# Kernel tuning notes

Measured on AMD Instinct MI355X. Metric: run time of the kernel, lower is better.

The kernel has to match this reference:

```python
import jax, jax.numpy as jnp
import numpy as np

B, N, C = 2, 4096, 1024
H, D = 16, 64
EPS = 1e-6


def setup_inputs() -> dict:
    key = jax.random.key(0)
    k1, k2, k3 = jax.random.split(key, 3)
    hidden_states = jax.random.normal(k1, (B, N, C), dtype=jnp.float32)
    # realistic RoPE tables: inv_freq over half-dim, duplicated to full head_dim
    half = D // 2
    inv_freq = 1.0 / (10000.0 ** (jnp.arange(half, dtype=jnp.float32) / half))
    t = jnp.arange(N, dtype=jnp.float32)
    freqs = jnp.outer(t, inv_freq)                     # [N, D/2]
    emb = jnp.concatenate([freqs, freqs], axis=-1)     # [N, D]
    cos, sin = jnp.cos(emb), jnp.sin(emb)
    Wqkv = jax.random.normal(k2, (C, 3 * C), dtype=jnp.float32) * (C ** -0.5)
    Wout = jax.random.normal(k3, (C, C), dtype=jnp.float32) * (C ** -0.5)
    gq = jnp.ones((D,), dtype=jnp.float32)
    gk = jnp.ones((D,), dtype=jnp.float32)
    return {"hidden_states": hidden_states, "cos": cos, "sin": sin,
            "Wqkv": Wqkv, "Wout": Wout, "gq": gq, "gk": gk}


def _rmsnorm(x, g):
    # normalize over last dim (head_dim)
    var = jnp.mean(jnp.square(x), axis=-1, keepdims=True)
    return x * jax.lax.rsqrt(var + EPS) * g


def _rotate_half(x):
    x1, x2 = jnp.split(x, 2, axis=-1)
    return jnp.concatenate([-x2, x1], axis=-1)


def reference(hidden_states, cos, sin, Wqkv, Wout, gq, gk):
    b, n, c = hidden_states.shape
    qkv = (hidden_states @ Wqkv).reshape(b, n, 3, H, D)
    qkv = jnp.transpose(qkv, (2, 0, 3, 1, 4))
    q, k, v = qkv[0], qkv[1], qkv[2]
    # per-head RMSNorm on q/k
    q = _rmsnorm(q, gq)
    k = _rmsnorm(k, gk)
    # RoPE: cos/sin [N,D] broadcast to [B,H,N,D]
    q = q * cos + _rotate_half(q) * sin
    k = k * cos + _rotate_half(k) * sin
    # full SDPA (flex_attention with no block_mask/score_mod)
    scale = D ** -0.5
    scores = jnp.einsum("bhqd,bhkd->bhqk", q, k) * scale
    probs = jax.nn.softmax(scores, axis=-1)
    attn = jnp.einsum("bhqk,bhkd->bhqd", probs, v)
    attn = jnp.transpose(attn, (0, 2, 1, 3)).reshape(b, n, c)
    return attn @ Wout
```

## Files before the change

### kernel.cpp

```cpp
#include <hip/hip_runtime.h>
#include <hip/hip_bf16.h>
#include <stdint.h>

#define LOG2E 1.44269504088896340736f

typedef __attribute__((ext_vector_type(8))) short short8;
typedef __attribute__((ext_vector_type(4))) float f32x4;
typedef __attribute__((ext_vector_type(16))) float f32x16;
typedef __attribute__((ext_vector_type(4))) unsigned short us4;

static __device__ __forceinline__ float bf2f(unsigned short u) {
    union { unsigned int i; float f; } v; v.i = ((unsigned int)u) << 16; return v.f;
}
static __device__ __forceinline__ unsigned short f2bf(float f) {
    __hip_bfloat16 h = __float2bfloat16(f);
    union { __hip_bfloat16 h; unsigned short u; } v; v.h = h; return v.u;
}

#define GLL(gsrc, ldst) \
    __builtin_amdgcn_global_load_lds((const __attribute__((address_space(1))) unsigned int*)(gsrc), \
                                     (__attribute__((address_space(3))) unsigned int*)(ldst), 16, 0, 0)

__global__ __launch_bounds__(256) void conv_bf16(const float4* __restrict__ in,
                                                 us4* __restrict__ out, int n4) {
    int i = blockIdx.x * blockDim.x + threadIdx.x;
    int stride = gridDim.x * blockDim.x;
    for (; i < n4; i += stride) {
        float4 v = in[i];
        us4 o;
        o[0] = f2bf(v.x); o[1] = f2bf(v.y); o[2] = f2bf(v.z); o[3] = f2bf(v.w);
        out[i] = o;
    }
}

__global__ __launch_bounds__(256) void transpose_w(const float* __restrict__ W,
                                                   unsigned short* __restrict__ WT,
                                                   int K, int M) {
    __shared__ unsigned short T[64][65];
    int m0 = blockIdx.x * 64, k0 = blockIdx.y * 64;
    int r = threadIdx.x >> 2, q = (threadIdx.x & 3) * 16;
    const float4* src = (const float4*)(W + (size_t)(k0 + r) * M + m0 + q);
#pragma unroll
    for (int j = 0; j < 4; j++) {
        float4 v = src[j];
        T[r][q + j * 4 + 0] = f2bf(v.x);
        T[r][q + j * 4 + 1] = f2bf(v.y);
        T[r][q + j * 4 + 2] = f2bf(v.z);
        T[r][q + j * 4 + 3] = f2bf(v.w);
    }
    __syncthreads();
    unsigned short tmp[16];
#pragma unroll
    for (int j = 0; j < 16; j++) tmp[j] = T[q + j][r];
    unsigned short* dst = WT + (size_t)(m0 + r) * K + k0 + q;
    *(short8*)dst = *(const short8*)tmp;
    *(short8*)(dst + 8) = *(const short8*)(tmp + 8);
}

__device__ __forceinline__ void gemm_core(const unsigned short* __restrict__ A,
                                          const unsigned short* __restrict__ Bt,
                                          int brow, int bcol,
                                          unsigned short* As, unsigned short* Bs,
                                          f32x4 (&acc)[4][4]) {
    const int tid = threadIdx.x;
    const int w = tid >> 6, lane = tid & 63;
    const int g = lane >> 4, c = lane & 15;
    const int wr = (w >> 1) * 64, wc = (w & 1) * 64;

    for (int k0 = 0; k0 < 1024; k0 += 64) {
        __syncthreads();
#pragma unroll
        for (int i = 0; i < 4; i++) {
            int slot = i * 256 + tid;
            int row = slot >> 3, sub = slot & 7;
            int koff = k0 + ((sub ^ (row & 7)) << 3);
            GLL(A + (size_t)(brow + row) * 1024 + koff, As + (size_t)(i * 256 + w * 64) * 8);
            GLL(Bt + (size_t)(bcol + row) * 1024 + koff, Bs + (size_t)(i * 256 + w * 64) * 8);
        }
        __syncthreads();
#pragma unroll
        for (int kc = 0; kc < 2; kc++) {
            short8 a[4], b[4];
#pragma unroll
            for (int f = 0; f < 4; f++) {
                int rowA = wr + f * 16 + c;
                a[f] = *(const short8*)(As + (size_t)(rowA * 8 + ((kc * 4 + g) ^ (rowA & 7))) * 8);
                int rowB = wc + f * 16 + c;
                b[f] = *(const short8*)(Bs + (size_t)(rowB * 8 + ((kc * 4 + g) ^ (rowB & 7))) * 8);
            }
#pragma unroll
            for (int fi = 0; fi < 4; fi++)
#pragma unroll
                for (int fj = 0; fj < 4; fj++)
                    acc[fi][fj] = __builtin_amdgcn_mfma_f32_16x16x32_bf16(a[fi], b[fj], acc[fi][fj], 0, 0, 0);
        }
    }
}

__global__ __launch_bounds__(256) void gemm_qkv(const unsigned short* __restrict__ A,
                                                const unsigned short* __restrict__ Bt,
                                                unsigned short* __restrict__ qkv,
                                                unsigned short* __restrict__ vt) {
    __shared__ unsigned short As[128 * 64];
    __shared__ unsigned short Bs[128 * 64];
    const int tid = threadIdx.x;
    const int lane = tid & 63, w = tid >> 6;
    const int g = lane >> 4, c = lane & 15;
    const int brow = blockIdx.x * 128, bcol = blockIdx.y * 128;
    const int wr = (w >> 1) * 64, wc = (w & 1) * 64;

    f32x4 acc[4][4];
#pragma unroll
    for (int i = 0; i < 4; i++)
#pragma unroll
        for (int j = 0; j < 4; j++) acc[i][j] = (f32x4){0.f, 0.f, 0.f, 0.f};

    gemm_core(A, Bt, brow, bcol, As, Bs, acc);

    if (bcol < 2048) {
#pragma unroll
        for (int fi = 0; fi < 4; fi++) {
            int row = brow + wr + fi * 16 + g * 4;
#pragma unroll
            for (int fj = 0; fj < 4; fj++) {
                int col = bcol + wc + fj * 16 + c;
#pragma unroll
                for (int r = 0; r < 4; r++)
                    qkv[(size_t)(row + r) * 2048 + col] = f2bf(acc[fi][fj][r]);
            }
        }
    } else {
        int b = brow >> 12;
        int nbase = (brow & 4095) + wr;
#pragma unroll
        for (int fi = 0; fi < 4; fi++) {
            int n0 = nbase + fi * 16 + g * 4;
#pragma unroll
            for (int fj = 0; fj < 4; fj++) {
                int hd = bcol - 2048 + wc + fj * 16 + c;
                us4 pk;
#pragma unroll
                for (int r = 0; r < 4; r++) pk[r] = f2bf(acc[fi][fj][r]);
                *(us4*)(vt + (size_t)(b * 1024 + hd) * 4096 + n0) = pk;
            }
        }
    }
}

__global__ __launch_bounds__(256) void gemm_out(const unsigned short* __restrict__ A,
                                                const unsigned short* __restrict__ Bt,
                                                float* __restrict__ C) {
    __shared__ unsigned short As[128 * 64];
    __shared__ unsigned short Bs[128 * 64];
    const int tid = threadIdx.x;
    const int lane = tid & 63, w = tid >> 6;
    const int g = lane >> 4, c = lane & 15;
    const int brow = blockIdx.x * 128, bcol = blockIdx.y * 128;
    const int wr = (w >> 1) * 64, wc = (w & 1) * 64;

    f32x4 acc[4][4];
#pragma unroll
    for (int i = 0; i < 4; i++)
#pragma unroll
        for (int j = 0; j < 4; j++) acc[i][j] = (f32x4){0.f, 0.f, 0.f, 0.f};

    gemm_core(A, Bt, brow, bcol, As, Bs, acc);

#pragma unroll
    for (int fi = 0; fi < 4; fi++) {
        int row = brow + wr + fi * 16 + g * 4;
#pragma unroll
        for (int fj = 0; fj < 4; fj++) {
            int col = bcol + wc + fj * 16 + c;
#pragma unroll
            for (int r = 0; r < 4; r++)
                C[(size_t)(row + r) * 1024 + col] = acc[fi][fj][r];
        }
    }
}

__global__ __launch_bounds__(256) void norm_rope(unsigned short* __restrict__ qkv,
                                                 const float* __restrict__ cosb,
                                                 const float* __restrict__ sinb,
                                                 const float* __restrict__ gq,
                                                 const float* __restrict__ gk) {
    int u = blockIdx.x * 4 + (threadIdx.x >> 6);
    int lane = threadIdx.x & 63;
    int t = u >> 5, rest = u & 31, h = rest >> 1, qk = rest & 1;
    int n = t & 4095;
    unsigned short* p = qkv + (size_t)t * 2048 + qk * 1024 + h * 64 + lane;
    float x = bf2f(*p);
    float ss = x * x;
#pragma unroll
    for (int m = 1; m < 64; m <<= 1) ss += __shfl_xor(ss, m, 64);
    float rr = rsqrtf(ss * 0.015625f + 1e-6f);
    float xn = x * rr * (qk ? gk[lane] : gq[lane]);
    float other = __shfl_xor(xn, 32, 64);
    float cv = cosb[n * 64 + lane], sv = sinb[n * 64 + lane];
    float rh = (lane < 32) ? -other : other;
    *p = f2bf(xn * cv + rh * sv);
}

__global__ __launch_bounds__(256, 2) void attn_fwd(const unsigned short* __restrict__ qkv,
                                                   const unsigned short* __restrict__ vt,
                                                   unsigned short* __restrict__ attn) {
    __shared__ unsigned short Ks[2][4096];
    __shared__ unsigned short Vs[2][4096];
    const int tid = threadIdx.x;
    const int w = tid >> 6, lane = tid & 63;
    const int c31 = lane & 31, hi = lane >> 5;

    int logical = (blockIdx.x & 7) * 64 + (blockIdx.x >> 3);
    const int bh = logical >> 4, qt = logical & 15;
    const int b = bh >> 4, h = bh & 15;
    const size_t tokbase = (size_t)b * 4096;
    const int q0 = qt * 256 + w * 64;

    short8 qf[2][4];
#pragma unroll
    for (int qs = 0; qs < 2; qs++)
#pragma unroll
        for (int sl = 0; sl < 4; sl++) {
            const unsigned short* src =
                qkv + (tokbase + q0 + qs * 32 + c31) * 2048 + h * 64 + sl * 16 + hi * 8;
            short8 v = *(const short8*)src;
#pragma unroll
            for (int j = 0; j < 8; j++)
                v[j] = (short)f2bf(bf2f((unsigned short)v[j]) * 0.125f);
            qf[qs][sl] = v;
        }

    f32x16 o[2][2];
#pragma unroll
    for (int qs = 0; qs < 2; qs++)
#pragma unroll
        for (int ds = 0; ds < 2; ds++)
#pragma unroll
            for (int r = 0; r < 16; r++) o[qs][ds][r] = 0.f;
    float m_run[2] = {-__builtin_inff(), -__builtin_inff()};
    float l_run[2] = {0.f, 0.f};

#define STAGE_KV(bi, kv0)                                                                     \
    {                                                                                          \
        _Pragma("unroll") for (int i = 0; i < 2; i++) {                                        \
            int s2 = i * 4 + w;                                                                \
            GLL(qkv + (tokbase + (kv0) + lane) * 2048 + 1024 + h * 64 + s2 * 8,                \
                &Ks[bi][(size_t)s2 * 512]);                                                    \
            GLL(vt + ((size_t)(bh * 64 + lane)) * 4096 + (kv0) + s2 * 8,                       \
                &Vs[bi][(size_t)s2 * 512]);                                                    \
        }                                                                                      \
    }

    STAGE_KV(0, 0);
    int cur = 0;

    for (int t = 0; t < 64; t++) {
        __syncthreads();
        if (t < 63) STAGE_KV(cur ^ 1, (t + 1) * 64);

        short8 kf[2][4];
#pragma unroll
        for (int m = 0; m < 2; m++)
#pragma unroll
            for (int sl = 0; sl < 4; sl++)
                kf[m][sl] = *(const short8*)&Ks[cur][(size_t)(((sl * 2 + hi) * 64) + m * 32 + c31) * 8];

        f32x16 sacc[2][2];
        __builtin_amdgcn_s_setprio(1);
#pragma unroll
        for (int qs = 0; qs < 2; qs++)
#pragma unroll
            for (int m = 0; m < 2; m++) {
                f32x16 a;
#pragma unroll
                for (int r = 0; r < 16; r++) a[r] = 0.f;
#pragma unroll
                for (int sl = 0; sl < 4; sl++)
                    a = __builtin_amdgcn_mfma_f32_32x32x16_bf16(kf[m][sl], qf[qs][sl], a, 0, 0, 0);
                sacc[qs][m] = a;
            }
        __builtin_amdgcn_s_setprio(0);

        short8 pf[2][4];
#pragma unroll
        for (int qs = 0; qs < 2; qs++) {
            f32x16 t16;
#pragma unroll
            for (int r = 0; r < 16; r++) t16[r] = fmaxf(sacc[qs][0][r], sacc[qs][1][r]);
#pragma unroll
            for (int st = 8; st > 0; st >>= 1)
#pragma unroll
                for (int j = 0; j < st; j++) t16[j] = fmaxf(t16[j], t16[j + st]);
            float mx = fmaxf(t16[0], __shfl_xor(t16[0], 32, 64));

            if (__any(mx > m_run[qs] + 4.0f)) {
                float mn = fmaxf(m_run[qs], mx);
                float alpha = __builtin_amdgcn_exp2f((m_run[qs] - mn) * LOG2E);
                m_run[qs] = mn;
                l_run[qs] *= alpha;
#pragma unroll
                for (int ds = 0; ds < 2; ds++)
#pragma unroll
                    for (int r = 0; r < 16; r++) o[qs][ds][r] *= alpha;
            }
            float nb = -m_run[qs] * LOG2E;

#pragma unroll
            for (int m = 0; m < 2; m++)
#pragma unroll
                for (int r = 0; r < 16; r++)
                    sacc[qs][m][r] = __builtin_amdgcn_exp2f(fmaf(sacc[qs][m][r], LOG2E, nb));

#pragma unroll
            for (int r = 0; r < 16; r++) t16[r] = sacc[qs][0][r] + sacc[qs][1][r];
#pragma unroll
            for (int st = 8; st > 0; st >>= 1)
#pragma unroll
                for (int j = 0; j < st; j++) t16[j] += t16[j + st];
            l_run[qs] += t16[0] + __shfl_xor(t16[0], 32, 64);

#pragma unroll
            for (int m = 0; m < 2; m++) {
                unsigned int q2[8];
#pragma unroll
                for (int w8 = 0; w8 < 8; w8++) {
                    unsigned int r_;
                    asm("v_cvt_pk_bf16_f32 %0, %1, %2"
                        : "=v"(r_)
                        : "v"(sacc[qs][m][2 * w8]), "v"(sacc[qs][m][2 * w8 + 1]));
                    q2[w8] = r_;
                }
                unsigned int x0 = hi ? q2[0] : q2[2];
                unsigned int x1 = hi ? q2[1] : q2[3];
                unsigned int x2 = hi ? q2[4] : q2[6];
                unsigned int x3 = hi ? q2[5] : q2[7];
                unsigned int r0 = (unsigned int)__shfl_xor((int)x0, 32, 64);
                unsigned int r1 = (unsigned int)__shfl_xor((int)x1, 32, 64);
                unsigned int r2 = (unsigned int)__shfl_xor((int)x2, 32, 64);
                unsigned int r3 = (unsigned int)__shfl_xor((int)x3, 32, 64);
                union { unsigned int u[4]; short8 s; } f0, f1;
                f0.u[0] = hi ? r0 : q2[0];
                f0.u[1] = hi ? r1 : q2[1];
                f0.u[2] = hi ? q2[2] : r0;
                f0.u[3] = hi ? q2[3] : r1;
                f1.u[0] = hi ? r2 : q2[4];
                f1.u[1] = hi ? r3 : q2[5];
                f1.u[2] = hi ? q2[6] : r2;
                f1.u[3] = hi ? q2[7] : r3;
                pf[qs][2 * m] = f0.s;
                pf[qs][2 * m + 1] = f1.s;
            }
        }

        __builtin_amdgcn_s_setprio(1);
#pragma unroll
        for (int ds = 0; ds < 2; ds++)
#pragma unroll
            for (int kvs = 0; kvs < 4; kvs++) {
                short8 vf = *(const short8*)&Vs[cur][(size_t)(((kvs * 2 + hi) * 64) + ds * 32 + c31) * 8];
                o[0][ds] = __builtin_amdgcn_mfma_f32_32x32x16_bf16(vf, pf[0][kvs], o[0][ds], 0, 0, 0);
                o[1][ds] = __builtin_amdgcn_mfma_f32_32x32x16_bf16(vf, pf[1][kvs], o[1][ds], 0, 0, 0);
            }
        __builtin_amdgcn_s_setprio(0);
        cur ^= 1;
    }

#pragma unroll
    for (int qs = 0; qs < 2; qs++) {
        float inv = 1.f / l_run[qs];
        int token = q0 + qs * 32 + c31;
#pragma unroll
        for (int ds = 0; ds < 2; ds++)
#pragma unroll
            for (int rb = 0; rb < 4; rb++) {
                us4 pk;
#pragma unroll
                for (int j = 0; j < 4; j++) pk[j] = f2bf(o[qs][ds][rb * 4 + j] * inv);
                *(us4*)(attn + (tokbase + token) * 1024 + h * 64 + ds * 32 + rb * 8 + hi * 4) = pk;
            }
    }
#undef STAGE_KV
}

extern "C" void kernel_launch(void* const* d_in, const int* in_sizes, int n_in,
                              void* d_out, int out_size, void* d_ws, size_t ws_size,
                              hipStream_t stream) {
    const float* hs   = (const float*)d_in[0];
    const float* cosb = (const float*)d_in[1];
    const float* sinb = (const float*)d_in[2];
    const float* wqkv = (const float*)d_in[3];
    const float* wout = (const float*)d_in[4];
    const float* gq   = (const float*)d_in[5];
    const float* gk   = (const float*)d_in[6];
    float* out = (float*)d_out;

    char* ws = (char*)d_ws;
    unsigned short* Xb    = (unsigned short*)(ws);
    unsigned short* WqkvT = (unsigned short*)(ws + 16777216);
    unsigned short* WoutT = (unsigned short*)(ws + 23068672);
    unsigned short* qkv   = (unsigned short*)(ws + 25165824);
    unsigned short* vt    = (unsigned short*)(ws + 58720256);
    unsigned short* attn  = (unsigned short*)(ws + 75497472);

    conv_bf16<<<4096, 256, 0, stream>>>((const float4*)hs, (us4*)Xb, (8192 * 1024) / 4);
    transpose_w<<<dim3(48, 16), 256, 0, stream>>>(wqkv, WqkvT, 1024, 3072);
    transpose_w<<<dim3(16, 16), 256, 0, stream>>>(wout, WoutT, 1024, 1024);
    gemm_qkv<<<dim3(64, 24), 256, 0, stream>>>(Xb, WqkvT, qkv, vt);
    norm_rope<<<65536, 256, 0, stream>>>(qkv, cosb, sinb, gq, gk);
    attn_fwd<<<512, 256, 0, stream>>>(qkv, vt, attn);
    gemm_out<<<dim3(64, 8), 256, 0, stream>>>(attn, WoutT, out);
}
```

Measured before the change: 419.1 us.

## Halve attention query tile per wave to double blocks and occupancy

Each wave now handles 32 query rows instead of 64, so a block covers 128 queries and the grid doubles to 1024 blocks, with launch bounds raised to 4 blocks per CU. The smaller per-wave state (Q fragments, O accumulators, scores) cuts register pressure so more waves can hide latency, and the larger grid fills the 256 CUs more evenly. In exchange, each staged K/V tile is reused by half as many queries, which doubles K/V global and LDS traffic per unit of compute and lowers MFMA work per LDS read.

```diff
diff --git a/kernel.cpp b/kernel.cpp
--- a/kernel.cpp
+++ b/kernel.cpp
@@ -201,7 +201,7 @@
     *p = f2bf(xn * cv + rh * sv);
 }
 
-__global__ __launch_bounds__(256, 2) void attn_fwd(const unsigned short* __restrict__ qkv,
+__global__ __launch_bounds__(256, 4) void attn_fwd(const unsigned short* __restrict__ qkv,
                                                    const unsigned short* __restrict__ vt,
                                                    unsigned short* __restrict__ attn) {
     __shared__ unsigned short Ks[2][4096];
@@ -210,35 +210,31 @@
     const int w = tid >> 6, lane = tid & 63;
     const int c31 = lane & 31, hi = lane >> 5;
 
-    int logical = (blockIdx.x & 7) * 64 + (blockIdx.x >> 3);
-    const int bh = logical >> 4, qt = logical & 15;
+    int logical = (blockIdx.x & 7) * 128 + (blockIdx.x >> 3);
+    const int bh = logical >> 5, qt = logical & 31;
     const int b = bh >> 4, h = bh & 15;
     const size_t tokbase = (size_t)b * 4096;
-    const int q0 = qt * 256 + w * 64;
-
-    short8 qf[2][4];
-#pragma unroll
-    for (int qs = 0; qs < 2; qs++)
-#pragma unroll
-        for (int sl = 0; sl < 4; sl++) {
-            const unsigned short* src =
-                qkv + (tokbase + q0 + qs * 32 + c31) * 2048 + h * 64 + sl * 16 + hi * 8;
-            short8 v = *(const short8*)src;
-#pragma unroll
-            for (int j = 0; j < 8; j++)
-                v[j] = (short)f2bf(bf2f((unsigned short)v[j]) * 0.125f);
-            qf[qs][sl] = v;
-        }
-
-    f32x16 o[2][2];
-#pragma unroll
-    for (int qs = 0; qs < 2; qs++)
-#pragma unroll
-        for (int ds = 0; ds < 2; ds++)
-#pragma unroll
-            for (int r = 0; r < 16; r++) o[qs][ds][r] = 0.f;
-    float m_run[2] = {-__builtin_inff(), -__builtin_inff()};
-    float l_run[2] = {0.f, 0.f};
+    const int q0 = qt * 128 + w * 32;
+
+    short8 qf[4];
+#pragma unroll
+    for (int sl = 0; sl < 4; sl++) {
+        const unsigned short* src =
+            qkv + (tokbase + q0 + c31) * 2048 + h * 64 + sl * 16 + hi * 8;
+        short8 v = *(const short8*)src;
+#pragma unroll
+        for (int j = 0; j < 8; j++)
+            v[j] = (short)f2bf(bf2f((unsigned short)v[j]) * 0.125f);
+        qf[sl] = v;
+    }
+
+    f32x16 o[2];
+#pragma unroll
+    for (int ds = 0; ds < 2; ds++)
+#pragma unroll
+        for (int r = 0; r < 16; r++) o[ds][r] = 0.f;
+    float m_run = -__builtin_inff();
+    float l_run = 0.f;
 
 #define STAGE_KV(bi, kv0)                                                                     \
     {                                                                                          \
@@ -265,59 +261,56 @@
             for (int sl = 0; sl < 4; sl++)
                 kf[m][sl] = *(const short8*)&Ks[cur][(size_t)(((sl * 2 + hi) * 64) + m * 32 + c31) * 8];
 
-        f32x16 sacc[2][2];
+        f32x16 sacc[2];
         __builtin_amdgcn_s_setprio(1);
 #pragma unroll
-        for (int qs = 0; qs < 2; qs++)
-#pragma unroll
-            for (int m = 0; m < 2; m++) {
-                f32x16 a;
-#pragma unroll
-                for (int r = 0; r < 16; r++) a[r] = 0.f;
-#pragma unroll
-                for (int sl = 0; sl < 4; sl++)
-                    a = __builtin_amdgcn_mfma_f32_32x32x16_bf16(kf[m][sl], qf[qs][sl], a, 0, 0, 0);
-                sacc[qs][m] = a;
-            }
+        for (int m = 0; m < 2; m++) {
+            f32x16 a;
+#pragma unroll
+            for (int r = 0; r < 16; r++) a[r] = 0.f;
+#pragma unroll
+            for (int sl = 0; sl < 4; sl++)
+                a = __builtin_amdgcn_mfma_f32_32x32x16_bf16(kf[m][sl], qf[sl], a, 0, 0, 0);
+            sacc[m] = a;
+        }
         __builtin_amdgcn_s_setprio(0);
 
-        short8 pf[2][4];
-#pragma unroll
-        for (int qs = 0; qs < 2; qs++) {
+        short8 pf[4];
+        {
             f32x16 t16;
 #pragma unroll
-            for (int r = 0; r < 16; r++) t16[r] = fmaxf(sacc[qs][0][r], sacc[qs][1][r]);
+            for (int r = 0; r < 16; r++) t16[r] = fmaxf(sacc[0][r], sacc[1][r]);
 #pragma unroll
             for (int st = 8; st > 0; st >>= 1)
 #pragma unroll
                 for (int j = 0; j < st; j++) t16[j] = fmaxf(t16[j], t16[j + st]);
             float mx = fmaxf(t16[0], __shfl_xor(t16[0], 32, 64));
 
-            if (__any(mx > m_run[qs] + 4.0f)) {
-                float mn = fmaxf(m_run[qs], mx);
-                float alpha = __builtin_amdgcn_exp2f((m_run[qs] - mn) * LOG2E);
-                m_run[qs] = mn;
-                l_run[qs] *= alpha;
+            if (__any(mx > m_run + 4.0f)) {
+                float mn = fmaxf(m_run, mx);
+                float alpha = __builtin_amdgcn_exp2f((m_run - mn) * LOG2E);
+                m_run = mn;
+                l_run *= alpha;
 #pragma unroll
                 for (int ds = 0; ds < 2; ds++)
 #pragma unroll
-                    for (int r = 0; r < 16; r++) o[qs][ds][r] *= alpha;
-            }
-            float nb = -m_run[qs] * LOG2E;
+                    for (int r = 0; r < 16; r++) o[ds][r] *= alpha;
+            }
+            float nb = -m_run * LOG2E;
 
 #pragma unroll
             for (int m = 0; m < 2; m++)
 #pragma unroll
                 for (int r = 0; r < 16; r++)
-                    sacc[qs][m][r] = __builtin_amdgcn_exp2f(fmaf(sacc[qs][m][r], LOG2E, nb));
-
-#pragma unroll
-            for (int r = 0; r < 16; r++) t16[r] = sacc[qs][0][r] + sacc[qs][1][r];
+                    sacc[m][r] = __builtin_amdgcn_exp2f(fmaf(sacc[m][r], LOG2E, nb));
+
+#pragma unroll
+            for (int r = 0; r < 16; r++) t16[r] = sacc[0][r] + sacc[1][r];
 #pragma unroll
             for (int st = 8; st > 0; st >>= 1)
 #pragma unroll
                 for (int j = 0; j < st; j++) t16[j] += t16[j + st];
-            l_run[qs] += t16[0] + __shfl_xor(t16[0], 32, 64);
+            l_run += t16[0] + __shfl_xor(t16[0], 32, 64);
 
 #pragma unroll
             for (int m = 0; m < 2; m++) {
@@ -327,7 +320,7 @@
                     unsigned int r_;
                     asm("v_cvt_pk_bf16_f32 %0, %1, %2"
                         : "=v"(r_)
-                        : "v"(sacc[qs][m][2 * w8]), "v"(sacc[qs][m][2 * w8 + 1]));
+                        : "v"(sacc[m][2 * w8]), "v"(sacc[m][2 * w8 + 1]));
                     q2[w8] = r_;
                 }
                 unsigned int x0 = hi ? q2[0] : q2[2];
@@ -347,8 +340,8 @@
                 f1.u[1] = hi ? r3 : q2[5];
                 f1.u[2] = hi ? q2[6] : r2;
                 f1.u[3] = hi ? q2[7] : r3;
-                pf[qs][2 * m] = f0.s;
-                pf[qs][2 * m + 1] = f1.s;
+                pf[2 * m] = f0.s;
+                pf[2 * m + 1] = f1.s;
             }
         }
 
@@ -358,24 +351,22 @@
 #pragma unroll
             for (int kvs = 0; kvs < 4; kvs++) {
                 short8 vf = *(const short8*)&Vs[cur][(size_t)(((kvs * 2 + hi) * 64) + ds * 32 + c31) * 8];
-                o[0][ds] = __builtin_amdgcn_mfma_f32_32x32x16_bf16(vf, pf[0][kvs], o[0][ds], 0, 0, 0);
-                o[1][ds] = __builtin_amdgcn_mfma_f32_32x32x16_bf16(vf, pf[1][kvs], o[1][ds], 0, 0, 0);
+                o[ds] = __builtin_amdgcn_mfma_f32_32x32x16_bf16(vf, pf[kvs], o[ds], 0, 0, 0);
             }
         __builtin_amdgcn_s_setprio(0);
         cur ^= 1;
     }
 
-#pragma unroll
-    for (int qs = 0; qs < 2; qs++) {
-        float inv = 1.f / l_run[qs];
-        int token = q0 + qs * 32 + c31;
+    {
+        float inv = 1.f / l_run;
+        int token = q0 + c31;
 #pragma unroll
         for (int ds = 0; ds < 2; ds++)
 #pragma unroll
             for (int rb = 0; rb < 4; rb++) {
                 us4 pk;
 #pragma unroll
-                for (int j = 0; j < 4; j++) pk[j] = f2bf(o[qs][ds][rb * 4 + j] * inv);
+                for (int j = 0; j < 4; j++) pk[j] = f2bf(o[ds][rb * 4 + j] * inv);
                 *(us4*)(attn + (tokbase + token) * 1024 + h * 64 + ds * 32 + rb * 8 + hi * 4) = pk;
             }
     }
@@ -407,6 +398,6 @@
     transpose_w<<<dim3(16, 16), 256, 0, stream>>>(wout, WoutT, 1024, 1024);
     gemm_qkv<<<dim3(64, 24), 256, 0, stream>>>(Xb, WqkvT, qkv, vt);
     norm_rope<<<65536, 256, 0, stream>>>(qkv, cosb, sinb, gq, gk);
-    attn_fwd<<<512, 256, 0, stream>>>(qkv, vt, attn);
+    attn_fwd<<<1024, 256, 0, stream>>>(qkv, vt, attn);
     gemm_out<<<dim3(64, 8), 256, 0, stream>>>(attn, WoutT, out);
 }
```

Result: no change. 416.7 us (-0.6%).
